# Kernel tuning notes

Hardware: AMD Instinct MI355X
Metric: run time of the kernel (lower is better)

The kernel has to match this reference:

```python
import jax, jax.numpy as jnp
import numpy as np

B, N, P, K = 128, 256, 256, 4  # batches, obs points, pred points, nfunc


def setup_inputs() -> dict:
    key = jax.random.key(0)
    k1, k2, k3, k4, k5 = jax.random.split(key, 5)
    # squared distances: symmetric obs-obs block with zero diagonal + obs-pred block
    d_oo = jax.random.uniform(k1, (B, N, N), dtype=jnp.float32) * 25.0
    d_oo = 0.5 * (d_oo + jnp.swapaxes(d_oo, -1, -2))
    d_oo = d_oo * (1.0 - jnp.eye(N, dtype=jnp.float32))
    d_op = jax.random.uniform(k2, (B, N, P), dtype=jnp.float32) * 25.0
    C = jnp.concatenate([d_oo, d_op], axis=-1)  # (B, N, N+P)
    val = jax.random.normal(k3, (B, N, K), dtype=jnp.float32)
    bad = jax.random.randint(k4, (B, N), 0, 10) == 0
    rm = jax.random.normal(k5, (K, 1), dtype=jnp.float32) * 0.1  # MyKF.rm param
    eps_param = -1.5 * jnp.ones((K,), dtype=jnp.float32)          # DistOA.eps param
    return {"C": C, "val": val, "rm": rm, "eps_param": eps_param, "bad": bad}


def _forward(C, val, rm, eps_param, bad):
    n = C.shape[-2]
    # MyKF: x = d2 * sigmoid(rm)/rmax^2 (rmax=1); kernel (1+x)exp(-x)  -> (K,B,n,n+p)
    rmk = jax.nn.sigmoid(rm)[..., None, None]            # (K,1,1,1)
    x = rmk * C[None]
    Cf = (1.0 + x) * jnp.exp(-x)                          # (K,B,n,n+p)
    b = Cf[..., n:]                                       # (K,B,n,p)
    Cm = Cf[..., :n]                                      # (K,B,n,n)
    # implicit: add sigmoid(eps) on the diagonal
    eps = jax.nn.sigmoid(eps_param)[:, None, None, None]  # (K,1,1,1)
    Cm = Cm + eps * jnp.eye(n, dtype=C.dtype)
    # NaN/bad masking: zero bad rows of b; zero xor(bad_i, bad_j) entries of C
    good = (~bad).astype(C.dtype)                         # (B,n)
    b = b * good[None, :, :, None]
    keep = (~(bad[:, :, None] ^ bad[:, None, :])).astype(C.dtype)  # (B,n,n)
    Cm = Cm * keep[None]
    # batched solve + clamp-based reweighting (edging=False)
    d = jnp.linalg.solve(Cm, b)                           # (K,B,n,p)
    wg = jnp.clip((jnp.abs(d).sum(-2, keepdims=True) - 1.0) * 2.0, 0.0, 1.0)
    d1 = b / Cm.sum(-1, keepdims=True)
    r = d * (1.0 - wg) + d1 * (wg / jnp.clip(d1.sum(-2, keepdims=True), 1.0, None))
    # neddvalgrad=False -> val detached before nan_to_num
    val0 = jnp.nan_to_num(jax.lax.stop_gradient(val))     # (B,n,K)
    return jnp.einsum('kbjp,bjk->bpk', r, val0)           # (B,p,K)


def reference(C, val, rm, eps_param, bad):
    return _forward(C, val, rm, eps_param, bad)
```

## Files before the change

kernel.cpp:

```cpp
#include <hip/hip_runtime.h>
#include <cstddef>

#define NN 256
#define PP 256
#define BB 128
#define KK 4
#define NSYS 512
#define PW 32
#define NPAN (NN/PW)

__device__ __forceinline__ float sigmoidf_(float x){ return 1.0f/(1.0f+expf(-x)); }

__global__ __launch_bounds__(256) void build_kernel(
    const float* __restrict__ C, const float* __restrict__ rm,
    const float* __restrict__ epsp, const int* __restrict__ bad,
    float* __restrict__ A, float* __restrict__ rowsum, int s0)
{
  const int si = blockIdx.x;
  const int ls = si >> 8;
  const int i  = si & 255;
  const int s  = s0 + ls;
  const int k  = s >> 7;
  const int b  = s & 127;
  const int j  = threadIdx.x;

  const float sk = sigmoidf_(rm[k]);
  const float ek = sigmoidf_(epsp[k]);
  const bool bad_i = bad[b*NN + i] != 0;
  const bool bad_j = bad[b*NN + j] != 0;

  float c  = C[((size_t)b*NN + i)*(NN+PP) + j];
  float x  = sk * c;
  float cf = (1.0f + x) * expf(-x);
  if (i == j) cf += ek;
  float keep = (bad_i == bad_j) ? 1.0f : 0.0f;
  float a = cf * keep;
  A[((size_t)ls*NN + i)*NN + j] = a;

  __shared__ float red[256];
  red[j] = a; __syncthreads();
  #pragma unroll
  for (int off = 128; off > 0; off >>= 1){
    if (j < off) red[j] += red[j + off];
    __syncthreads();
  }
  if (j == 0) rowsum[ls*NN + i] = red[0];
}

__global__ __launch_bounds__(512, 4) void lu_kernel(
    float* __restrict__ Aall, int* __restrict__ permAll)
{
  __shared__ float panel[NN][PW+1];
  __shared__ float linv[PW][PW+1];
  __shared__ float uinv[PW][PW+1];
  __shared__ float urow[PW][NN-PW];
  __shared__ float redv[2][8];
  __shared__ int   redi[2][8];
  __shared__ int   pivseq[NN];
  __shared__ int   actlist[NN];
  __shared__ unsigned char pickedsh[NN];
  __shared__ int   nact;

  const int ls = blockIdx.x;
  float* __restrict__ A = Aall + (size_t)ls*NN*NN;
  const int t = threadIdx.x;
  const int lane = t & 63, wid = t >> 6;
  bool picked = false;
  if (t < NN) pickedsh[t] = 0;

  for (int I = 0; I < NPAN; ++I){
    const int col0 = I*PW;
    const int W = NN - col0 - PW;
    if (t == 0) nact = 0;
    __syncthreads();

    for (int e = t; e < NN*PW; e += 512){
      int r = e >> 5, c = e & 31;
      panel[r][c] = A[(size_t)r*NN + col0 + c];
    }
    __syncthreads();

    {
      float v = -1.0f; int vi = 0;
      if (t < NN && !picked){ v = fabsf(panel[t][0]); vi = t; }
      #pragma unroll
      for (int off = 32; off > 0; off >>= 1){
        float ov = __shfl_down(v, off); int oi = __shfl_down(vi, off);
        if (ov > v){ v = ov; vi = oi; }
      }
      if (lane == 0){ redv[0][wid] = v; redi[0][wid] = vi; }
    }
    __syncthreads();

    for (int c = 0; c < PW; ++c){
      const int par = c & 1;
      float bv = redv[par][0]; int p = redi[par][0];
      #pragma unroll
      for (int w = 1; w < 8; ++w)
        if (redv[par][w] > bv){ bv = redv[par][w]; p = redi[par][w]; }
      if (t == p){ picked = true; pickedsh[t] = 1; pivseq[col0+c] = t; }

      float nv = -1.0f; int ni = t;
      if (t < NN && !picked){
        const float rdia = 1.0f / panel[p][c];
        float m = panel[t][c] * rdia;
        panel[t][c] = m;
        float nxt = -1.0f;
        #pragma unroll
        for (int j = 0; j < PW; ++j){
          if (j > c){
            float u = panel[t][j] - m * panel[p][j];
            panel[t][j] = u;
            if (j == c+1) nxt = fabsf(u);
          }
        }
        nv = nxt;
      }
      #pragma unroll
      for (int off = 32; off > 0; off >>= 1){
        float ov = __shfl_down(nv, off); int oi = __shfl_down(ni, off);
        if (ov > nv){ nv = ov; ni = oi; }
      }
      if (lane == 0){ redv[par^1][wid] = nv; redi[par^1][wid] = ni; }
      __syncthreads();
    }

    if (t >= 256){
      const int jj = t - 256;
      if (jj < W){
        const int j = col0 + PW + jj;
        float u[PW];
        #pragma unroll
        for (int c = 0; c < PW; ++c) u[c] = A[(size_t)pivseq[col0+c]*NN + j];
        #pragma unroll
        for (int c = 0; c < PW; ++c){
          const int pc = pivseq[col0+c];
          float sv = u[c];
          #pragma unroll
          for (int k2 = 0; k2 < PW; ++k2)
            if (k2 < c) sv -= panel[pc][k2] * u[k2];
          u[c] = sv;
          urow[c][jj] = sv;
          A[(size_t)pc*NN + j] = sv;
        }
      }
    } else if (t < PW){
      const int cth = t;
      for (int r = cth; r < PW; ++r){
        float sv = (r == cth) ? 1.0f : 0.0f;
        const int pr = pivseq[col0+r];
        for (int k2 = cth; k2 < r; ++k2) sv -= panel[pr][k2] * linv[k2][cth];
        linv[r][cth] = sv;
      }
    } else if (t >= 64 && t < 64+PW){
      const int cth = t - 64;
      for (int r = cth; r >= 0; --r){
        float sv = (r == cth) ? 1.0f : 0.0f;
        const int pr = pivseq[col0+r];
        for (int k2 = r+1; k2 <= cth; ++k2) sv -= panel[pr][k2] * uinv[k2][cth];
        uinv[r][cth] = sv / panel[pr][r];
      }
    } else if (t >= 128 && t < 192){
      #pragma unroll
      for (int q = 0; q < 4; ++q){
        int r = (t-128)*4 + q;
        if (!pickedsh[r]){ int pos = atomicAdd(&nact, 1); actlist[pos] = r; }
      }
    }
    __syncthreads();

    for (int e = t; e < PW*PW; e += 512){
      int r = e >> 5, c2 = e & 31;
      A[(size_t)pivseq[col0+r]*NN + col0 + c2] = (r > c2) ? linv[r][c2] : uinv[r][c2];
    }
    for (int e = t; e < NN*PW; e += 512){
      int r = e >> 5, c2 = e & 31;
      if (!pickedsh[r]) A[(size_t)r*NN + col0 + c2] = panel[r][c2];
    }

    if (W > 0){
      for (int i0 = wid*2; i0 < W; i0 += 16){
        const int r0 = actlist[i0];
        const int r1 = actlist[i0+1];
        float4* R0 = (float4*)(A + (size_t)r0*NN + col0 + PW);
        float4* R1 = (float4*)(A + (size_t)r1*NN + col0 + PW);
        if (lane*4 < W){
          float4 a0 = R0[lane];
          float4 a1 = R1[lane];
          #pragma unroll
          for (int c = 0; c < PW; ++c){
            float4 u4 = *(const float4*)&urow[c][lane*4];
            float p0 = panel[r0][c], p1 = panel[r1][c];
            a0.x -= p0*u4.x; a0.y -= p0*u4.y; a0.z -= p0*u4.z; a0.w -= p0*u4.w;
            a1.x -= p1*u4.x; a1.y -= p1*u4.y; a1.z -= p1*u4.z; a1.w -= p1*u4.w;
          }
          R0[lane] = a0;
          R1[lane] = a1;
        }
      }
    }
  }
  __syncthreads();
  if (t < NN) permAll[ls*NN + t] = pivseq[t];
}

__global__ __launch_bounds__(512) void solve_epi_kernel(
    const float* __restrict__ Aall, const int* __restrict__ permAll,
    const float* __restrict__ rowsum,
    const float* __restrict__ C, const float* __restrict__ val,
    const int* __restrict__ bad, const float* __restrict__ rm,
    float* __restrict__ out, int s0)
{
  __shared__ float tile[NN][64];
  __shared__ float dblk[PW][PW+1];
  __shared__ __align__(16) float ubuf[2048];
  __shared__ int   perm[NN];

  int ls, c0;
  {
    const int g = blockIdx.x;
    if ((gridDim.x & 31) == 0){
      const int xcd = g & 7, idx = g >> 3;
      ls = xcd + 8*(idx >> 2);
      c0 = (idx & 3) * 64;
    } else {
      ls = g >> 2;
      c0 = (g & 3) * 64;
    }
  }
  const int s  = s0 + ls;
  const int k  = s >> 7, b = s & 127;
  const float* __restrict__ A = Aall + (size_t)ls*NN*NN;
  const float* __restrict__ rs = rowsum + ls*NN;
  const int t = threadIdx.x;
  const int lane = t & 63, wid = t >> 6;
  const float sk = sigmoidf_(rm[k]);

  if (t < NN) perm[t] = permAll[ls*NN + t];
  __syncthreads();

  for (int e = t; e < NN*64; e += 512){
    int i = e >> 6, c = e & 63;
    int pi = perm[i];
    float cb = C[((size_t)b*NN + pi)*(NN+PP) + NN + c0 + c];
    float xb = sk * cb;
    float bf = (1.0f + xb) * expf(-xb);
    if (bad[b*NN + pi]) bf = 0.0f;
    tile[i][c] = bf;
  }
  __syncthreads();

  for (int J = 0; J < NPAN; ++J){
    const int j0 = J*PW;
    for (int e = t; e < PW*PW; e += 512){
      int r = e >> 5, c = e & 31;
      dblk[r][c] = A[(size_t)perm[j0+r]*NN + j0 + c];
    }
    __syncthreads();
    const int r0 = wid*4;
    float y0 = tile[j0+r0+0][lane];
    float y1 = tile[j0+r0+1][lane];
    float y2 = tile[j0+r0+2][lane];
    float y3 = tile[j0+r0+3][lane];
    for (int kk = 0; kk < r0; ++kk){
      float xk = tile[j0+kk][lane];
      y0 += dblk[r0+0][kk]*xk;
      y1 += dblk[r0+1][kk]*xk;
      y2 += dblk[r0+2][kk]*xk;
      y3 += dblk[r0+3][kk]*xk;
    }
    {
      float x0 = tile[j0+r0][lane], x1 = tile[j0+r0+1][lane], x2 = tile[j0+r0+2][lane];
      y1 += dblk[r0+1][r0]*x0;
      y2 += dblk[r0+2][r0]*x0 + dblk[r0+2][r0+1]*x1;
      y3 += dblk[r0+3][r0]*x0 + dblk[r0+3][r0+1]*x1 + dblk[r0+3][r0+2]*x2;
    }
    __syncthreads();
    tile[j0+r0+0][lane]=y0; tile[j0+r0+1][lane]=y1;
    tile[j0+r0+2][lane]=y2; tile[j0+r0+3][lane]=y3;
    __syncthreads();
    if (j0 + PW < NN){
      float x[PW];
      #pragma unroll
      for (int kk = 0; kk < PW; ++kk) x[kk] = tile[j0+kk][lane];
      const int nbelow = NN - j0 - PW;
      for (int cb2 = 0; cb2 < nbelow; cb2 += 64){
        const int rows_c = (nbelow - cb2 < 64) ? (nbelow - cb2) : 64;
        if (t < rows_c*8){
          int lr = t >> 3, q = t & 7;
          *(float4*)&ubuf[(lr<<5) + (q<<2)] =
            *(const float4*)(A + (size_t)perm[j0+PW+cb2+lr]*NN + j0 + (q<<2));
        }
        __syncthreads();
        const int rpw = rows_c >> 3;
        for (int p2 = 0; p2 < rpw; p2 += 2){
          const int lr0 = wid*rpw + p2;
          const int ia = j0 + PW + cb2 + lr0, ib = ia + 1;
          const float* __restrict__ S0 = &ubuf[lr0<<5];
          const float* __restrict__ S1 = &ubuf[(lr0+1)<<5];
          float acc0 = tile[ia][lane];
          float acc1 = tile[ib][lane];
          #pragma unroll
          for (int q = 0; q < 8; ++q){
            float4 a4 = *(const float4*)(S0 + (q<<2));
            float4 b4 = *(const float4*)(S1 + (q<<2));
            acc0 -= a4.x*x[q*4+0] + a4.y*x[q*4+1] + a4.z*x[q*4+2] + a4.w*x[q*4+3];
            acc1 -= b4.x*x[q*4+0] + b4.y*x[q*4+1] + b4.z*x[q*4+2] + b4.w*x[q*4+3];
          }
          tile[ia][lane] = acc0;
          tile[ib][lane] = acc1;
        }
        __syncthreads();
      }
    }
  }

  for (int J = NPAN-1; J >= 0; --J){
    const int j0 = J*PW;
    for (int e = t; e < PW*PW; e += 512){
      int r = e >> 5, c = e & 31;
      dblk[r][c] = A[(size_t)perm[j0+r]*NN + j0 + c];
    }
    __syncthreads();
    const int r0 = wid*4;
    float y0=0.f, y1=0.f, y2=0.f, y3=0.f;
    for (int kk = r0+4; kk < PW; ++kk){
      float xk = tile[j0+kk][lane];
      y0 += dblk[r0+0][kk]*xk;
      y1 += dblk[r0+1][kk]*xk;
      y2 += dblk[r0+2][kk]*xk;
      y3 += dblk[r0+3][kk]*xk;
    }
    {
      float x0 = tile[j0+r0][lane], x1 = tile[j0+r0+1][lane];
      float x2 = tile[j0+r0+2][lane], x3 = tile[j0+r0+3][lane];
      y0 += dblk[r0][r0]*x0 + dblk[r0][r0+1]*x1 + dblk[r0][r0+2]*x2 + dblk[r0][r0+3]*x3;
      y1 += dblk[r0+1][r0+1]*x1 + dblk[r0+1][r0+2]*x2 + dblk[r0+1][r0+3]*x3;
      y2 += dblk[r0+2][r0+2]*x2 + dblk[r0+2][r0+3]*x3;
      y3 += dblk[r0+3][r0+3]*x3;
    }
    __syncthreads();
    tile[j0+r0+0][lane]=y0; tile[j0+r0+1][lane]=y1;
    tile[j0+r0+2][lane]=y2; tile[j0+r0+3][lane]=y3;
    __syncthreads();
    if (j0 > 0){
      float x[PW];
      #pragma unroll
      for (int kk = 0; kk < PW; ++kk) x[kk] = tile[j0+kk][lane];
      for (int cb2 = 0; cb2 < j0; cb2 += 64){
        const int rows_c = (j0 - cb2 < 64) ? (j0 - cb2) : 64;
        if (t < rows_c*8){
          int lr = t >> 3, q = t & 7;
          *(float4*)&ubuf[(lr<<5) + (q<<2)] =
            *(const float4*)(A + (size_t)perm[cb2+lr]*NN + j0 + (q<<2));
        }
        __syncthreads();
        const int rpw = rows_c >> 3;
        for (int p2 = 0; p2 < rpw; p2 += 2){
          const int lr0 = wid*rpw + p2;
          const int ia = cb2 + lr0, ib = ia + 1;
          const float* __restrict__ S0 = &ubuf[lr0<<5];
          const float* __restrict__ S1 = &ubuf[(lr0+1)<<5];
          float acc0 = tile[ia][lane];
          float acc1 = tile[ib][lane];
          #pragma unroll
          for (int q = 0; q < 8; ++q){
            float4 a4 = *(const float4*)(S0 + (q<<2));
            float4 b4 = *(const float4*)(S1 + (q<<2));
            acc0 -= a4.x*x[q*4+0] + a4.y*x[q*4+1] + a4.z*x[q*4+2] + a4.w*x[q*4+3];
            acc1 -= b4.x*x[q*4+0] + b4.y*x[q*4+1] + b4.z*x[q*4+2] + b4.w*x[q*4+3];
          }
          tile[ia][lane] = acc0;
          tile[ib][lane] = acc1;
        }
        __syncthreads();
      }
    }
  }

  {
    const int p = c0 + lane;
    float sdv=0.f, sabs=0.f, s1v=0.f, s1=0.f;
    for (int j = wid*32; j < wid*32 + 32; ++j){
      float d = tile[j][lane];
      float v = val[(b*NN + j)*KK + k];
      if (v != v) v = 0.0f;
      float cb = C[((size_t)b*NN + j)*(NN+PP) + NN + p];
      float xb = sk*cb;
      float bo = (1.0f+xb)*expf(-xb);
      if (bad[b*NN + j]) bo = 0.0f;
      float d1 = bo / rs[j];
      sdv += d*v; sabs += fabsf(d); s1v += d1*v; s1 += d1;
    }
    __syncthreads();
    ubuf[( 0 + wid)*64 + lane] = sdv;
    ubuf[( 8 + wid)*64 + lane] = sabs;
    ubuf[(16 + wid)*64 + lane] = s1v;
    ubuf[(24 + wid)*64 + lane] = s1;
  }
  __syncthreads();
  if (t < 64){
    float sdv=0.f, sabs=0.f, s1v=0.f, s1=0.f;
    #pragma unroll
    for (int w = 0; w < 8; ++w){
      sdv  += ubuf[( 0 + w)*64 + lane];
      sabs += ubuf[( 8 + w)*64 + lane];
      s1v  += ubuf[(16 + w)*64 + lane];
      s1   += ubuf[(24 + w)*64 + lane];
    }
    float wg    = fminf(fmaxf((sabs - 1.0f)*2.0f, 0.0f), 1.0f);
    float denom = fmaxf(s1, 1.0f);
    out[((size_t)b*PP + c0 + lane)*KK + k] = (1.0f - wg)*sdv + (wg/denom)*s1v;
  }
}

extern "C" void kernel_launch(void* const* d_in, const int* in_sizes, int n_in,
                              void* d_out, int out_size, void* d_ws, size_t ws_size,
                              hipStream_t stream)
{
  (void)in_sizes; (void)n_in; (void)out_size;
  const float* C    = (const float*)d_in[0];
  const float* val  = (const float*)d_in[1];
  const float* rm   = (const float*)d_in[2];
  const float* epsp = (const float*)d_in[3];
  const int*   bad  = (const int*)d_in[4];
  float* out = (float*)d_out;

  const size_t per_sys = (size_t)NN*NN*4 + (size_t)NN*4 + (size_t)NN*4;
  int chunk = (int)(ws_size / per_sys);
  if (chunk < 1)    chunk = 1;
  if (chunk > NSYS) chunk = NSYS;

  float* ws     = (float*)d_ws;
  float* A      = ws;
  float* rowsum = A + (size_t)chunk*NN*NN;
  int*   perm   = (int*)(rowsum + (size_t)chunk*NN);

  for (int s0 = 0; s0 < NSYS; s0 += chunk){
    int cs = (NSYS - s0 < chunk) ? (NSYS - s0) : chunk;
    build_kernel<<<cs*NN, 256, 0, stream>>>(C, rm, epsp, bad, A, rowsum, s0);
    lu_kernel<<<cs, 512, 0, stream>>>(A, perm);
    solve_epi_kernel<<<cs*4, 512, 0, stream>>>(A, perm, rowsum, C, val, bad, rm, out, s0);
  }
}
```

Baseline: 1.745 ms.

## Widen solve tile to 128 RHS columns per block to reuse L/U loads

Each solve_epi block now handles 128 right-hand-side columns instead of 64, with every thread processing two columns. This halves the grid and halves the redundant global reads of the factored matrix panels and permutation per system, and lets each LDS-loaded coefficient feed twice as many FMAs. In exchange, LDS use roughly doubles (tile 128KB plus a larger ubuf), which cuts occupancy to one block per CU, and the doubled x arrays raise register pressure. The grid also shrinks to 1024 blocks.

Result: faster. 1.530 ms (median of 2 runs) (-12.4%).

```diff
diff --git a/kernel.cpp b/kernel.cpp
--- a/kernel.cpp
+++ b/kernel.cpp
@@ -211,21 +211,21 @@
     const int* __restrict__ bad, const float* __restrict__ rm,
     float* __restrict__ out, int s0)
 {
-  __shared__ float tile[NN][64];
+  __shared__ float tile[NN][128];
   __shared__ float dblk[PW][PW+1];
-  __shared__ __align__(16) float ubuf[2048];
+  __shared__ __align__(16) float ubuf[4096];
   __shared__ int   perm[NN];
 
   int ls, c0;
   {
     const int g = blockIdx.x;
-    if ((gridDim.x & 31) == 0){
+    if ((gridDim.x & 15) == 0){
       const int xcd = g & 7, idx = g >> 3;
-      ls = xcd + 8*(idx >> 2);
-      c0 = (idx & 3) * 64;
+      ls = xcd + 8*(idx >> 1);
+      c0 = (idx & 1) * 128;
     } else {
-      ls = g >> 2;
-      c0 = (g & 3) * 64;
+      ls = g >> 1;
+      c0 = (g & 1) * 128;
     }
   }
   const int s  = s0 + ls;
@@ -234,13 +234,16 @@
   const float* __restrict__ rs = rowsum + ls*NN;
   const int t = threadIdx.x;
   const int lane = t & 63, wid = t >> 6;
+  const int lane2 = lane + 64;
   const float sk = sigmoidf_(rm[k]);
+  const int slr = t >> 3;
+  const int sq4 = (t & 7) << 2;
 
   if (t < NN) perm[t] = permAll[ls*NN + t];
   __syncthreads();
 
-  for (int e = t; e < NN*64; e += 512){
-    int i = e >> 6, c = e & 63;
+  for (int e = t; e < NN*128; e += 512){
+    int i = e >> 7, c = e & 127;
     int pi = perm[i];
     float cb = C[((size_t)b*NN + pi)*(NN+PP) + NN + c0 + c];
     float xb = sk * cb;
@@ -258,39 +261,44 @@
     }
     __syncthreads();
     const int r0 = wid*4;
-    float y0 = tile[j0+r0+0][lane];
-    float y1 = tile[j0+r0+1][lane];
-    float y2 = tile[j0+r0+2][lane];
-    float y3 = tile[j0+r0+3][lane];
+    float ya0 = tile[j0+r0+0][lane],  yb0 = tile[j0+r0+0][lane2];
+    float ya1 = tile[j0+r0+1][lane],  yb1 = tile[j0+r0+1][lane2];
+    float ya2 = tile[j0+r0+2][lane],  yb2 = tile[j0+r0+2][lane2];
+    float ya3 = tile[j0+r0+3][lane],  yb3 = tile[j0+r0+3][lane2];
     for (int kk = 0; kk < r0; ++kk){
-      float xk = tile[j0+kk][lane];
-      y0 += dblk[r0+0][kk]*xk;
-      y1 += dblk[r0+1][kk]*xk;
-      y2 += dblk[r0+2][kk]*xk;
-      y3 += dblk[r0+3][kk]*xk;
+      float xa = tile[j0+kk][lane], xb = tile[j0+kk][lane2];
+      float d0 = dblk[r0+0][kk], d1 = dblk[r0+1][kk], d2 = dblk[r0+2][kk], d3 = dblk[r0+3][kk];
+      ya0 += d0*xa; yb0 += d0*xb;
+      ya1 += d1*xa; yb1 += d1*xb;
+      ya2 += d2*xa; yb2 += d2*xb;
+      ya3 += d3*xa; yb3 += d3*xb;
     }
     {
-      float x0 = tile[j0+r0][lane], x1 = tile[j0+r0+1][lane], x2 = tile[j0+r0+2][lane];
-      y1 += dblk[r0+1][r0]*x0;
-      y2 += dblk[r0+2][r0]*x0 + dblk[r0+2][r0+1]*x1;
-      y3 += dblk[r0+3][r0]*x0 + dblk[r0+3][r0+1]*x1 + dblk[r0+3][r0+2]*x2;
-    }
-    __syncthreads();
-    tile[j0+r0+0][lane]=y0; tile[j0+r0+1][lane]=y1;
-    tile[j0+r0+2][lane]=y2; tile[j0+r0+3][lane]=y3;
-    __syncthreads();
-    if (j0 + PW < NN){
-      float x[PW];
-      #pragma unroll
-      for (int kk = 0; kk < PW; ++kk) x[kk] = tile[j0+kk][lane];
-      const int nbelow = NN - j0 - PW;
+      float xa0 = tile[j0+r0][lane],  xa1 = tile[j0+r0+1][lane],  xa2 = tile[j0+r0+2][lane];
+      float xb0 = tile[j0+r0][lane2], xb1 = tile[j0+r0+1][lane2], xb2 = tile[j0+r0+2][lane2];
+      float e10 = dblk[r0+1][r0];
+      float e20 = dblk[r0+2][r0], e21 = dblk[r0+2][r0+1];
+      float e30 = dblk[r0+3][r0], e31 = dblk[r0+3][r0+1], e32 = dblk[r0+3][r0+2];
+      ya1 += e10*xa0;                         yb1 += e10*xb0;
+      ya2 += e20*xa0 + e21*xa1;               yb2 += e20*xb0 + e21*xb1;
+      ya3 += e30*xa0 + e31*xa1 + e32*xa2;     yb3 += e30*xb0 + e31*xb1 + e32*xb2;
+    }
+    __syncthreads();
+    tile[j0+r0+0][lane]=ya0; tile[j0+r0+0][lane2]=yb0;
+    tile[j0+r0+1][lane]=ya1; tile[j0+r0+1][lane2]=yb1;
+    tile[j0+r0+2][lane]=ya2; tile[j0+r0+2][lane2]=yb2;
+    tile[j0+r0+3][lane]=ya3; tile[j0+r0+3][lane2]=yb3;
+    __syncthreads();
+    const int nbelow = NN - j0 - PW;
+    if (nbelow > 0){
+      float xa[PW], xb[PW];
+      #pragma unroll
+      for (int kk = 0; kk < PW; ++kk){ xa[kk] = tile[j0+kk][lane]; xb[kk] = tile[j0+kk][lane2]; }
       for (int cb2 = 0; cb2 < nbelow; cb2 += 64){
         const int rows_c = (nbelow - cb2 < 64) ? (nbelow - cb2) : 64;
-        if (t < rows_c*8){
-          int lr = t >> 3, q = t & 7;
-          *(float4*)&ubuf[(lr<<5) + (q<<2)] =
-            *(const float4*)(A + (size_t)perm[j0+PW+cb2+lr]*NN + j0 + (q<<2));
-        }
+        if (t < rows_c*8)
+          *(float4*)&ubuf[(slr<<5) + sq4] =
+            *(const float4*)(A + (size_t)perm[j0+PW+cb2+slr]*NN + j0 + sq4);
         __syncthreads();
         const int rpw = rows_c >> 3;
         for (int p2 = 0; p2 < rpw; p2 += 2){
@@ -298,17 +306,19 @@
           const int ia = j0 + PW + cb2 + lr0, ib = ia + 1;
           const float* __restrict__ S0 = &ubuf[lr0<<5];
           const float* __restrict__ S1 = &ubuf[(lr0+1)<<5];
-          float acc0 = tile[ia][lane];
-          float acc1 = tile[ib][lane];
+          float a0a = tile[ia][lane], a0b = tile[ia][lane2];
+          float a1a = tile[ib][lane], a1b = tile[ib][lane2];
           #pragma unroll
           for (int q = 0; q < 8; ++q){
             float4 a4 = *(const float4*)(S0 + (q<<2));
             float4 b4 = *(const float4*)(S1 + (q<<2));
-            acc0 -= a4.x*x[q*4+0] + a4.y*x[q*4+1] + a4.z*x[q*4+2] + a4.w*x[q*4+3];
-            acc1 -= b4.x*x[q*4+0] + b4.y*x[q*4+1] + b4.z*x[q*4+2] + b4.w*x[q*4+3];
+            a0a -= a4.x*xa[q*4+0] + a4.y*xa[q*4+1] + a4.z*xa[q*4+2] + a4.w*xa[q*4+3];
+            a0b -= a4.x*xb[q*4+0] + a4.y*xb[q*4+1] + a4.z*xb[q*4+2] + a4.w*xb[q*4+3];
+            a1a -= b4.x*xa[q*4+0] + b4.y*xa[q*4+1] + b4.z*xa[q*4+2] + b4.w*xa[q*4+3];
+            a1b -= b4.x*xb[q*4+0] + b4.y*xb[q*4+1] + b4.z*xb[q*4+2] + b4.w*xb[q*4+3];
           }
-          tile[ia][lane] = acc0;
-          tile[ib][lane] = acc1;
+          tile[ia][lane] = a0a; tile[ia][lane2] = a0b;
+          tile[ib][lane] = a1a; tile[ib][lane2] = a1b;
         }
         __syncthreads();
       }
@@ -323,37 +333,45 @@
     }
     __syncthreads();
     const int r0 = wid*4;
-    float y0=0.f, y1=0.f, y2=0.f, y3=0.f;
+    float ya0=0.f, ya1=0.f, ya2=0.f, ya3=0.f;
+    float yb0=0.f, yb1=0.f, yb2=0.f, yb3=0.f;
     for (int kk = r0+4; kk < PW; ++kk){
-      float xk = tile[j0+kk][lane];
-      y0 += dblk[r0+0][kk]*xk;
-      y1 += dblk[r0+1][kk]*xk;
-      y2 += dblk[r0+2][kk]*xk;
-      y3 += dblk[r0+3][kk]*xk;
+      float xa = tile[j0+kk][lane], xb = tile[j0+kk][lane2];
+      float d0 = dblk[r0+0][kk], d1 = dblk[r0+1][kk], d2 = dblk[r0+2][kk], d3 = dblk[r0+3][kk];
+      ya0 += d0*xa; yb0 += d0*xb;
+      ya1 += d1*xa; yb1 += d1*xb;
+      ya2 += d2*xa; yb2 += d2*xb;
+      ya3 += d3*xa; yb3 += d3*xb;
     }
     {
-      float x0 = tile[j0+r0][lane], x1 = tile[j0+r0+1][lane];
-      float x2 = tile[j0+r0+2][lane], x3 = tile[j0+r0+3][lane];
-      y0 += dblk[r0][r0]*x0 + dblk[r0][r0+1]*x1 + dblk[r0][r0+2]*x2 + dblk[r0][r0+3]*x3;
-      y1 += dblk[r0+1][r0+1]*x1 + dblk[r0+1][r0+2]*x2 + dblk[r0+1][r0+3]*x3;
-      y2 += dblk[r0+2][r0+2]*x2 + dblk[r0+2][r0+3]*x3;
-      y3 += dblk[r0+3][r0+3]*x3;
-    }
-    __syncthreads();
-    tile[j0+r0+0][lane]=y0; tile[j0+r0+1][lane]=y1;
-    tile[j0+r0+2][lane]=y2; tile[j0+r0+3][lane]=y3;
+      float xa0 = tile[j0+r0][lane],  xa1 = tile[j0+r0+1][lane];
+      float xa2 = tile[j0+r0+2][lane], xa3 = tile[j0+r0+3][lane];
+      float xb0 = tile[j0+r0][lane2],  xb1 = tile[j0+r0+1][lane2];
+      float xb2 = tile[j0+r0+2][lane2], xb3 = tile[j0+r0+3][lane2];
+      float e00=dblk[r0][r0], e01=dblk[r0][r0+1], e02=dblk[r0][r0+2], e03=dblk[r0][r0+3];
+      float e11=dblk[r0+1][r0+1], e12=dblk[r0+1][r0+2], e13=dblk[r0+1][r0+3];
+      float e22=dblk[r0+2][r0+2], e23=dblk[r0+2][r0+3];
+      float e33=dblk[r0+3][r0+3];
+      ya0 += e00*xa0 + e01*xa1 + e02*xa2 + e03*xa3;  yb0 += e00*xb0 + e01*xb1 + e02*xb2 + e03*xb3;
+      ya1 += e11*xa1 + e12*xa2 + e13*xa3;            yb1 += e11*xb1 + e12*xb2 + e13*xb3;
+      ya2 += e22*xa2 + e23*xa3;                      yb2 += e22*xb2 + e23*xb3;
+      ya3 += e33*xa3;                                yb3 += e33*xb3;
+    }
+    __syncthreads();
+    tile[j0+r0+0][lane]=ya0; tile[j0+r0+0][lane2]=yb0;
+    tile[j0+r0+1][lane]=ya1; tile[j0+r0+1][lane2]=yb1;
+    tile[j0+r0+2][lane]=ya2; tile[j0+r0+2][lane2]=yb2;
+    tile[j0+r0+3][lane]=ya3; tile[j0+r0+3][lane2]=yb3;
     __syncthreads();
     if (j0 > 0){
-      float x[PW];
-      #pragma unroll
-      for (int kk = 0; kk < PW; ++kk) x[kk] = tile[j0+kk][lane];
+      float xa[PW], xb[PW];
+      #pragma unroll
+      for (int kk = 0; kk < PW; ++kk){ xa[kk] = tile[j0+kk][lane]; xb[kk] = tile[j0+kk][lane2]; }
       for (int cb2 = 0; cb2 < j0; cb2 += 64){
         const int rows_c = (j0 - cb2 < 64) ? (j0 - cb2) : 64;
-        if (t < rows_c*8){
-          int lr = t >> 3, q = t & 7;
-          *(float4*)&ubuf[(lr<<5) + (q<<2)] =
-            *(const float4*)(A + (size_t)perm[cb2+lr]*NN + j0 + (q<<2));
-        }
+        if (t < rows_c*8)
+          *(float4*)&ubuf[(slr<<5) + sq4] =
+            *(const float4*)(A + (size_t)perm[cb2+slr]*NN + j0 + sq4);
         __syncthreads();
         const int rpw = rows_c >> 3;
         for (int p2 = 0; p2 < rpw; p2 += 2){
@@ -361,17 +379,19 @@
           const int ia = cb2 + lr0, ib = ia + 1;
           const float* __restrict__ S0 = &ubuf[lr0<<5];
           const float* __restrict__ S1 = &ubuf[(lr0+1)<<5];
-          float acc0 = tile[ia][lane];
-          float acc1 = tile[ib][lane];
+          float a0a = tile[ia][lane], a0b = tile[ia][lane2];
+          float a1a = tile[ib][lane], a1b = tile[ib][lane2];
           #pragma unroll
           for (int q = 0; q < 8; ++q){
             float4 a4 = *(const float4*)(S0 + (q<<2));
             float4 b4 = *(const float4*)(S1 + (q<<2));
-            acc0 -= a4.x*x[q*4+0] + a4.y*x[q*4+1] + a4.z*x[q*4+2] + a4.w*x[q*4+3];
-            acc1 -= b4.x*x[q*4+0] + b4.y*x[q*4+1] + b4.z*x[q*4+2] + b4.w*x[q*4+3];
+            a0a -= a4.x*xa[q*4+0] + a4.y*xa[q*4+1] + a4.z*xa[q*4+2] + a4.w*xa[q*4+3];
+            a0b -= a4.x*xb[q*4+0] + a4.y*xb[q*4+1] + a4.z*xb[q*4+2] + a4.w*xb[q*4+3];
+            a1a -= b4.x*xa[q*4+0] + b4.y*xa[q*4+1] + b4.z*xa[q*4+2] + b4.w*xa[q*4+3];
+            a1b -= b4.x*xb[q*4+0] + b4.y*xb[q*4+1] + b4.z*xb[q*4+2] + b4.w*xb[q*4+3];
           }
-          tile[ia][lane] = acc0;
-          tile[ib][lane] = acc1;
+          tile[ia][lane] = a0a; tile[ia][lane2] = a0b;
+          tile[ib][lane] = a1a; tile[ib][lane2] = a1b;
         }
         __syncthreads();
       }
@@ -379,38 +399,48 @@
   }
 
   {
-    const int p = c0 + lane;
-    float sdv=0.f, sabs=0.f, s1v=0.f, s1=0.f;
+    float sdva=0.f, sabsa=0.f, s1va=0.f, s1a=0.f;
+    float sdvb=0.f, sabsb=0.f, s1vb=0.f, s1b=0.f;
+    const int pa = c0 + lane, pb = c0 + lane2;
     for (int j = wid*32; j < wid*32 + 32; ++j){
-      float d = tile[j][lane];
       float v = val[(b*NN + j)*KK + k];
       if (v != v) v = 0.0f;
-      float cb = C[((size_t)b*NN + j)*(NN+PP) + NN + p];
-      float xb = sk*cb;
-      float bo = (1.0f+xb)*expf(-xb);
-      if (bad[b*NN + j]) bo = 0.0f;
-      float d1 = bo / rs[j];
-      sdv += d*v; sabs += fabsf(d); s1v += d1*v; s1 += d1;
-    }
-    __syncthreads();
-    ubuf[( 0 + wid)*64 + lane] = sdv;
-    ubuf[( 8 + wid)*64 + lane] = sabs;
-    ubuf[(16 + wid)*64 + lane] = s1v;
-    ubuf[(24 + wid)*64 + lane] = s1;
+      const float rsj = rs[j];
+      const bool bj = bad[b*NN + j] != 0;
+      float da = tile[j][lane];
+      float cba = C[((size_t)b*NN + j)*(NN+PP) + NN + pa];
+      float xba = sk*cba;
+      float boa = (1.0f+xba)*expf(-xba);
+      if (bj) boa = 0.0f;
+      float d1a = boa / rsj;
+      sdva += da*v; sabsa += fabsf(da); s1va += d1a*v; s1a += d1a;
+      float db = tile[j][lane2];
+      float cbb = C[((size_t)b*NN + j)*(NN+PP) + NN + pb];
+      float xbb = sk*cbb;
+      float bob = (1.0f+xbb)*expf(-xbb);
+      if (bj) bob = 0.0f;
+      float d1b = bob / rsj;
+      sdvb += db*v; sabsb += fabsf(db); s1vb += d1b*v; s1b += d1b;
+    }
+    __syncthreads();
+    ubuf[(0*8 + wid)*128 + lane] = sdva;  ubuf[(0*8 + wid)*128 + lane2] = sdvb;
+    ubuf[(1*8 + wid)*128 + lane] = sabsa; ubuf[(1*8 + wid)*128 + lane2] = sabsb;
+    ubuf[(2*8 + wid)*128 + lane] = s1va;  ubuf[(2*8 + wid)*128 + lane2] = s1vb;
+    ubuf[(3*8 + wid)*128 + lane] = s1a;   ubuf[(3*8 + wid)*128 + lane2] = s1b;
   }
   __syncthreads();
-  if (t < 64){
+  if (t < 128){
     float sdv=0.f, sabs=0.f, s1v=0.f, s1=0.f;
     #pragma unroll
     for (int w = 0; w < 8; ++w){
-      sdv  += ubuf[( 0 + w)*64 + lane];
-      sabs += ubuf[( 8 + w)*64 + lane];
-      s1v  += ubuf[(16 + w)*64 + lane];
-      s1   += ubuf[(24 + w)*64 + lane];
+      sdv  += ubuf[(0*8 + w)*128 + t];
+      sabs += ubuf[(1*8 + w)*128 + t];
+      s1v  += ubuf[(2*8 + w)*128 + t];
+      s1   += ubuf[(3*8 + w)*128 + t];
     }
     float wg    = fminf(fmaxf((sabs - 1.0f)*2.0f, 0.0f), 1.0f);
     float denom = fmaxf(s1, 1.0f);
-    out[((size_t)b*PP + c0 + lane)*KK + k] = (1.0f - wg)*sdv + (wg/denom)*s1v;
+    out[((size_t)b*PP + c0 + t)*KK + k] = (1.0f - wg)*sdv + (wg/denom)*s1v;
   }
 }
 
@@ -440,6 +470,6 @@
     int cs = (NSYS - s0 < chunk) ? (NSYS - s0) : chunk;
     build_kernel<<<cs*NN, 256, 0, stream>>>(C, rm, epsp, bad, A, rowsum, s0);
     lu_kernel<<<cs, 512, 0, stream>>>(A, perm);
-    solve_epi_kernel<<<cs*4, 512, 0, stream>>>(A, perm, rowsum, C, val, bad, rm, out, s0);
+    solve_epi_kernel<<<cs*2, 512, 0, stream>>>(A, perm, rowsum, C, val, bad, rm, out, s0);
   }
 }
```
